# Kernel tuning notes

Measured on AMD Instinct MI355X. Metric: run time of the kernel, lower is better.

Reference implementation:

```python
import jax, jax.numpy as jnp
import numpy as np

# Scalar quantization params (QLinear __init__ args)
FEATURE_BITWIDTH = 8
WEIGHT_BITWIDTH = 8
INPUT_ZERO_POINT = -3
OUTPUT_ZERO_POINT = -5
INPUT_SCALE = 0.05
OUTPUT_SCALE = 0.1
QMIN = -(1 << (FEATURE_BITWIDTH - 1))   # -128
QMAX = (1 << (FEATURE_BITWIDTH - 1)) - 1  # 127

M, K, N = 8192, 4096, 4096


def float_to_fixed_point(x, bitwidth):
    """Represent x (0 < x < 1) as int_scale * 2^-frac_bits with int_scale
    in [2^(bitwidth-2), 2^(bitwidth-1)) (mantissa fits in signed `bitwidth` bits)."""
    frac_bits = (bitwidth - 1 - jnp.ceil(jnp.log2(x))).astype(jnp.int32)
    int_scale = jnp.round(x * jnp.exp2(frac_bits.astype(jnp.float32))).astype(jnp.int32)
    return int_scale, frac_bits


def setup_inputs() -> dict:
    key = jax.random.key(0)
    k1, k2, k3, k4 = jax.random.split(key, 4)
    qinput = jax.random.randint(k1, (M, K), -128, 128, dtype=jnp.int8)
    qweight = jax.random.randint(k2, (N, K), -128, 128, dtype=jnp.int8)
    qbias = jax.random.randint(k3, (N,), -(1 << 16), 1 << 16, dtype=jnp.int32)
    # per-output-channel weight scale; keeps folded scale in (0, 1)
    weight_scale = jax.random.uniform(k4, (N,), jnp.float32, 0.002, 0.02)
    return {"qinput": qinput, "qweight": qweight, "qbias": qbias,
            "weight_scale": weight_scale}


def reference(qinput, qweight, qbias, weight_scale):
    w32 = qweight.astype(jnp.int32)                      # [N, K]
    # Qbias' = qbias - sum_k(qweight) * Zin  (bias shift folding input zero point)
    shifted_qbias = qbias - w32.sum(axis=1) * INPUT_ZERO_POINT  # [N]
    # int32 GEMM: [M, K] @ [K, N] + bias
    acc = qinput.astype(jnp.int32) @ w32.T + shifted_qbias[None, :]  # [M, N]
    # fixed-point requantization: (acc * int_scale) >> frac_bits + Zout
    folded_scale = INPUT_SCALE * weight_scale / OUTPUT_SCALE         # [N], in (0,1)
    int_scale, frac_bits = float_to_fixed_point(folded_scale, FEATURE_BITWIDTH)
    # widen to int64 for the multiply so the (acc * int_scale) product cannot wrap
    prod = acc.astype(jnp.int64) * int_scale.astype(jnp.int64)[None, :]
    scaled = jnp.right_shift(prod, frac_bits.astype(jnp.int64)[None, :])  # arithmetic >>
    out = scaled + OUTPUT_ZERO_POINT
    return jnp.clip(out, QMIN, QMAX).astype(jnp.int8)
```

## Files before the change

kernel.cpp:

```cpp
#include <hip/hip_runtime.h>
#include <cstdint>
#include <cstddef>

#define M_DIM 8192
#define N_DIM 4096
#define K_DIM 4096

#define BM 128
#define BN 128
#define BK 128

typedef int int32x4 __attribute__((ext_vector_type(4)));


typedef __attribute__((address_space(1))) const void* gas_cptr;
typedef __attribute__((address_space(3))) void* las_ptr;

__device__ __forceinline__ void async_copy16(const void* g, void* l) {
    __builtin_amdgcn_global_load_lds((gas_cptr)g, (las_ptr)l, 16, 0, 0);
}

__device__ __forceinline__ int32x4 pack16(const int* p) {
    const int32x4* v = (const int32x4*)p;
    int32x4 w0 = v[0], w1 = v[1], w2 = v[2], w3 = v[3];
    int32x4 r;
    r.x = (w0.x & 0xFF) | ((w0.y & 0xFF) << 8) | ((w0.z & 0xFF) << 16) | (w0.w << 24);
    r.y = (w1.x & 0xFF) | ((w1.y & 0xFF) << 8) | ((w1.z & 0xFF) << 16) | (w1.w << 24);
    r.z = (w2.x & 0xFF) | ((w2.y & 0xFF) << 8) | ((w2.z & 0xFF) << 16) | (w2.w << 24);
    r.w = (w3.x & 0xFF) | ((w3.y & 0xFF) << 8) | ((w3.z & 0xFF) << 16) | (w3.w << 24);
    return r;
}

__global__ void ql_detect_kernel(const int* a, const int* b, int* ws) {
    int t = threadIdx.x;
    int fa = 0, fb = 0;
    for (int i = t; i < 4096; i += 64) {
        int va = a[i]; if (va > 127 || va < -128) fa = 1;
        int vb = b[i]; if (vb > 127 || vb < -128) fb = 1;
    }
    unsigned long long ba = __ballot(fa);
    unsigned long long bb = __ballot(fb);
    if (t == 0) { ws[0] = ba ? 1 : 0; ws[1] = bb ? 1 : 0; }
}

__global__ __launch_bounds__(256)
void ql_pack_all_kernel(const void* asrc, const void* bsrc, int* adst, int* bdst,
                        int* ws) {
    const int fa = __builtin_amdgcn_readfirstlane(ws[0]);
    const int fb = __builtin_amdgcn_readfirstlane(ws[1]);
    const int t    = threadIdx.x;
    const int lane = t & 63;
    const int wid  = t >> 6;

    if (blockIdx.x < N_DIM / 4) {
        const int n = blockIdx.x * 4 + wid;
        int s = 0;
        if (fb) {
            const int* src = (const int*)bsrc + (size_t)n * (K_DIM / 4);
#pragma unroll
            for (int it = 0; it < 4; ++it) {
                const int c = it * 64 + lane;
                int w = src[c];
                bdst[(size_t)n * (K_DIM / 4) + c] = w;
                s += (int)(int8_t)(w) + (int)(int8_t)(w >> 8)
                   + (int)(int8_t)(w >> 16) + (w >> 24);
            }
        } else {
            const int32x4* src = (const int32x4*)bsrc + (size_t)n * (K_DIM / 4);
#pragma unroll
            for (int it = 0; it < 16; ++it) {
                const int c = it * 64 + lane;
                int32x4 v = src[c];
                int w = (v.x & 0xFF) | ((v.y & 0xFF) << 8)
                      | ((v.z & 0xFF) << 16) | (v.w << 24);
                bdst[(size_t)n * (K_DIM / 4) + c] = w;
                s += v.x + v.y + v.z + v.w;
            }
        }
#pragma unroll
        for (int off = 32; off > 0; off >>= 1) s += __shfl_down(s, off, 64);
        if (lane == 0) ws[16 + n] = s;
    } else {
        const long base = (long)(blockIdx.x - N_DIM / 4) * 1024;
        if (fa) {
#pragma unroll
            for (int it = 0; it < 4; ++it) {
                const long c = base + it * 256 + t;
                adst[c] = ((const int*)asrc)[c];
            }
        } else {
#pragma unroll
            for (int it = 0; it < 4; ++it) {
                const long c = base + it * 256 + t;
                int32x4 v = ((const int32x4*)asrc)[c];
                adst[c] = (v.x & 0xFF) | ((v.y & 0xFF) << 8)
                        | ((v.z & 0xFF) << 16) | (v.w << 24);
            }
        }
    }
}

__device__ __forceinline__ int acc_elem(const int32x4& a, int r) {
    return (r == 0) ? a.x : (r == 1) ? a.y : (r == 2) ? a.z : a.w;
}

__device__ __forceinline__ void ql_epilogue(int32x4 acc[4][4], const int* rs,
                                            const int* qbias, const float* wscale,
                                            int* out, int bm, int bn,
                                            int wm, int wn, int qm, int qh) {
#pragma unroll
    for (int j = 0; j < 4; ++j) {
        const int n_g = bn * BN + wn + j * 16 + qm;
        const int b0 = qbias[n_g] + 3 * rs[n_g];
        float folded = (0.05f * wscale[n_g]) / 0.1f;
        const int f0 = (int)(7.0f - ceilf(log2f(folded)));
        const int s0 = (int)rintf(folded * exp2f((float)f0));
#pragma unroll
        for (int i = 0; i < 4; ++i) {
            const int m_base = bm * BM + wm + i * 16 + qh * 4;
#pragma unroll
            for (int r = 0; r < 4; ++r) {
                int v = acc_elem(acc[i][j], r) + b0;
                long long p = (long long)v * (long long)s0;
                int o = (int)(p >> f0) - 5;
                o = o < -128 ? -128 : (o > 127 ? 127 : o);
                out[(size_t)(m_base + r) * N_DIM + n_g] = o;
            }
        }
    }
}

__global__ __launch_bounds__(256)
void ql_gemm_kernel(const int8_t* aptr, const int8_t* bptr, const int* ws,
                    const int* qbias, const float* wscale, int* out) {
    __shared__ int32x4 Als[BM * BK / 16];
    __shared__ int32x4 Bls[BN * BK / 16];

    const int t    = threadIdx.x;
    const int lane = t & 63;
    const int wid  = t >> 6;
    const int bm = blockIdx.x;
    const int bn = blockIdx.y;

    const int wm = (wid >> 1) * 64;
    const int wn = (wid & 1) * 64;
    const int qm = lane & 15;
    const int qh = lane >> 4;

    int32x4 acc[4][4] = {};

    for (int kt = 0; kt < K_DIM / BK; ++kt) {
        __syncthreads();
        const int k0 = kt * BK;
#pragma unroll
        for (int r = 0; r < 4; ++r) {
            const int c    = r * 256 + t;
            const int row  = c >> 3;
            const int colg = (c & 7) ^ (row & 7);
            const size_t offA = (size_t)(bm * BM + row) * K_DIM + k0 + colg * 16;
            const size_t offB = (size_t)(bn * BN + row) * K_DIM + k0 + colg * 16;
            async_copy16(aptr + offA, &Als[c]);
            async_copy16(bptr + offB, &Bls[c]);
        }
        __syncthreads();

#pragma unroll
        for (int s = 0; s < 2; ++s) {
            const int colk = s * 4 + qh;
            int32x4 af[4], bf[4];
#pragma unroll
            for (int i = 0; i < 4; ++i) {
                const int ra = wm + i * 16 + qm;
                const int rb = wn + i * 16 + qm;
                af[i] = Als[ra * 8 + (colk ^ (ra & 7))];
                bf[i] = Bls[rb * 8 + (colk ^ (rb & 7))];
            }
#pragma unroll
            for (int i = 0; i < 4; ++i)
#pragma unroll
                for (int j = 0; j < 4; ++j)
                    acc[i][j] = __builtin_amdgcn_mfma_i32_16x16x64_i8(
                        af[i], bf[j], acc[i][j], 0, 0, 0);
        }
    }
    ql_epilogue(acc, ws + 16, qbias, wscale, out, bm, bn, wm, wn, qm, qh);
}

__global__ void ql_prep_kernel(const void* wptr, int* ws) {
    const int lane = threadIdx.x & 63;
    const int wid  = threadIdx.x >> 6;
    const int n = blockIdx.x * 4 + wid;
    const int b8 = __builtin_amdgcn_readfirstlane(ws[1]);

    int s = 0;
    if (b8) {
        const int32x4* row = (const int32x4*)((const int8_t*)wptr + (size_t)n * K_DIM);
        for (int c = lane; c < K_DIM / 16; c += 64) {
            int32x4 v = row[c];
#pragma unroll
            for (int j = 0; j < 4; ++j) {
                int w = (j == 0) ? v.x : (j == 1) ? v.y : (j == 2) ? v.z : v.w;
                s += (int)(int8_t)(w) + (int)(int8_t)(w >> 8)
                   + (int)(int8_t)(w >> 16) + (w >> 24);
            }
        }
    } else {
        const int32x4* row = (const int32x4*)((const int*)wptr + (size_t)n * K_DIM);
        for (int c = lane; c < K_DIM / 4; c += 64) {
            int32x4 v = row[c];
            s += v.x + v.y + v.z + v.w;
        }
    }
#pragma unroll
    for (int off = 32; off > 0; off >>= 1) s += __shfl_down(s, off, 64);
    if (lane == 0) ws[16 + n] = s;
}

__global__ __launch_bounds__(256)
void ql_gemm_fb_kernel(const void* aptr, const void* bptr, const int* ws,
                       const int* qbias, const float* wscale, int* out) {
    __shared__ int32x4 Als[BM * BK / 16];
    __shared__ int32x4 Bls[BN * BK / 16];

    const int a8 = __builtin_amdgcn_readfirstlane(ws[0]);
    const int b8 = __builtin_amdgcn_readfirstlane(ws[1]);

    const int t    = threadIdx.x;
    const int lane = t & 63;
    const int wid  = t >> 6;
    const int bm = blockIdx.x;
    const int bn = blockIdx.y;

    const int wm = (wid >> 1) * 64;
    const int wn = (wid & 1) * 64;
    const int qm = lane & 15;
    const int qh = lane >> 4;

    int32x4 acc[4][4] = {};

    for (int kt = 0; kt < K_DIM / BK; ++kt) {
        __syncthreads();
        const int k0 = kt * BK;
#pragma unroll
        for (int r = 0; r < 4; ++r) {
            const int c    = r * 256 + t;
            const int row  = c >> 3;
            const int colg = (c & 7) ^ (row & 7);
            const size_t offA = (size_t)(bm * BM + row) * K_DIM + k0 + colg * 16;
            const size_t offB = (size_t)(bn * BN + row) * K_DIM + k0 + colg * 16;
            if (a8) async_copy16((const int8_t*)aptr + offA, &Als[c]);
            else    Als[c] = pack16((const int*)aptr + offA);
            if (b8) async_copy16((const int8_t*)bptr + offB, &Bls[c]);
            else    Bls[c] = pack16((const int*)bptr + offB);
        }
        __syncthreads();

#pragma unroll
        for (int s = 0; s < 2; ++s) {
            const int colk = s * 4 + qh;
            int32x4 af[4], bf[4];
#pragma unroll
            for (int i = 0; i < 4; ++i) {
                const int ra = wm + i * 16 + qm;
                const int rb = wn + i * 16 + qm;
                af[i] = Als[ra * 8 + (colk ^ (ra & 7))];
                bf[i] = Bls[rb * 8 + (colk ^ (rb & 7))];
            }
#pragma unroll
            for (int i = 0; i < 4; ++i)
#pragma unroll
                for (int j = 0; j < 4; ++j)
                    acc[i][j] = __builtin_amdgcn_mfma_i32_16x16x64_i8(
                        af[i], bf[j], acc[i][j], 0, 0, 0);
        }
    }
    ql_epilogue(acc, ws + 16, qbias, wscale, out, bm, bn, wm, wn, qm, qh);
}

extern "C" void kernel_launch(void* const* d_in, const int* in_sizes, int n_in,
                              void* d_out, int out_size, void* d_ws, size_t ws_size,
                              hipStream_t stream) {
    const void* qin    = d_in[0];
    const void* qwt    = d_in[1];
    const int* qbias   = (const int*)d_in[2];
    const float* wscal = (const float*)d_in[3];
    int* ws  = (int*)d_ws;
    int* out = (int*)d_out;

    hipLaunchKernelGGL(ql_detect_kernel, dim3(1), dim3(64), 0, stream,
                       (const int*)qin, (const int*)qwt, ws);

    const size_t need = 65536 + (size_t)M_DIM * K_DIM + (size_t)N_DIM * K_DIM;
    if (ws_size >= need) {
        int8_t* a8 = (int8_t*)d_ws + 65536;
        int8_t* w8 = a8 + (size_t)M_DIM * K_DIM;
        const unsigned packGrid = N_DIM / 4 + (unsigned)((size_t)M_DIM * K_DIM / 4096);
        hipLaunchKernelGGL(ql_pack_all_kernel, dim3(packGrid), dim3(256), 0, stream,
                           qin, qwt, (int*)a8, (int*)w8, ws);
        hipLaunchKernelGGL(ql_gemm_kernel, dim3(M_DIM / BM, N_DIM / BN), dim3(256),
                           0, stream, a8, w8, ws, qbias, wscal, out);
    } else {
        hipLaunchKernelGGL(ql_prep_kernel, dim3(N_DIM / 4), dim3(256), 0, stream,
                           qwt, ws);
        hipLaunchKernelGGL(ql_gemm_fb_kernel, dim3(M_DIM / BM, N_DIM / BN), dim3(256),
                           0, stream, qin, qwt, ws, qbias, wscal, out);
    }
}
```

Baseline: 475.4 us.

## Switch main GEMM to 32x32x32 int8 MFMA and swap grid order

The main GEMM kernel now uses the 32x32x32 int8 MFMA with 2x2 accumulator tiles per wave instead of 4x4 tiles of 16x16x64. This halves the LDS fragment loads per MFMA and changes the register layout, so the epilogue is rewritten for the 32x32 output mapping. The grid is also transposed so consecutive blocks walk along N, which changes L2 reuse of the A rows. The larger MFMA may have different issue and latency characteristics, and the epilogue store pattern changes.

```diff
diff --git a/kernel.cpp b/kernel.cpp
--- a/kernel.cpp
+++ b/kernel.cpp
@@ -10,7 +10,8 @@
 #define BN 128
 #define BK 128
 
-typedef int int32x4 __attribute__((ext_vector_type(4)));
+typedef int int32x4  __attribute__((ext_vector_type(4)));
+typedef int int32x16 __attribute__((ext_vector_type(16)));
 
 
 typedef __attribute__((address_space(1))) const void* gas_cptr;
@@ -100,34 +101,8 @@
     }
 }
 
-__device__ __forceinline__ int acc_elem(const int32x4& a, int r) {
+__device__ __forceinline__ int acc_elem4(const int32x4& a, int r) {
     return (r == 0) ? a.x : (r == 1) ? a.y : (r == 2) ? a.z : a.w;
-}
-
-__device__ __forceinline__ void ql_epilogue(int32x4 acc[4][4], const int* rs,
-                                            const int* qbias, const float* wscale,
-                                            int* out, int bm, int bn,
-                                            int wm, int wn, int qm, int qh) {
-#pragma unroll
-    for (int j = 0; j < 4; ++j) {
-        const int n_g = bn * BN + wn + j * 16 + qm;
-        const int b0 = qbias[n_g] + 3 * rs[n_g];
-        float folded = (0.05f * wscale[n_g]) / 0.1f;
-        const int f0 = (int)(7.0f - ceilf(log2f(folded)));
-        const int s0 = (int)rintf(folded * exp2f((float)f0));
-#pragma unroll
-        for (int i = 0; i < 4; ++i) {
-            const int m_base = bm * BM + wm + i * 16 + qh * 4;
-#pragma unroll
-            for (int r = 0; r < 4; ++r) {
-                int v = acc_elem(acc[i][j], r) + b0;
-                long long p = (long long)v * (long long)s0;
-                int o = (int)(p >> f0) - 5;
-                o = o < -128 ? -128 : (o > 127 ? 127 : o);
-                out[(size_t)(m_base + r) * N_DIM + n_g] = o;
-            }
-        }
-    }
 }
 
 __global__ __launch_bounds__(256)
@@ -139,15 +114,16 @@
     const int t    = threadIdx.x;
     const int lane = t & 63;
     const int wid  = t >> 6;
-    const int bm = blockIdx.x;
-    const int bn = blockIdx.y;
+    const int bn = blockIdx.x;
+    const int bm = blockIdx.y;
 
     const int wm = (wid >> 1) * 64;
     const int wn = (wid & 1) * 64;
-    const int qm = lane & 15;
-    const int qh = lane >> 4;
-
-    int32x4 acc[4][4] = {};
+    const int l31 = lane & 31;
+    const int lh  = lane >> 5;
+    const int l7  = lane & 7;
+
+    int32x16 acc[2][2] = {};
 
     for (int kt = 0; kt < K_DIM / BK; ++kt) {
         __syncthreads();
@@ -165,25 +141,47 @@
         __syncthreads();
 
 #pragma unroll
-        for (int s = 0; s < 2; ++s) {
-            const int colk = s * 4 + qh;
-            int32x4 af[4], bf[4];
-#pragma unroll
-            for (int i = 0; i < 4; ++i) {
-                const int ra = wm + i * 16 + qm;
-                const int rb = wn + i * 16 + qm;
-                af[i] = Als[ra * 8 + (colk ^ (ra & 7))];
-                bf[i] = Bls[rb * 8 + (colk ^ (rb & 7))];
-            }
-#pragma unroll
-            for (int i = 0; i < 4; ++i)
-#pragma unroll
-                for (int j = 0; j < 4; ++j)
-                    acc[i][j] = __builtin_amdgcn_mfma_i32_16x16x64_i8(
+        for (int ks = 0; ks < 4; ++ks) {
+            const int colk = ks * 2 + lh;
+            int32x4 af[2], bf[2];
+#pragma unroll
+            for (int i = 0; i < 2; ++i) {
+                const int ra = wm + i * 32 + l31;
+                const int rb = wn + i * 32 + l31;
+                af[i] = Als[ra * 8 + (colk ^ l7)];
+                bf[i] = Bls[rb * 8 + (colk ^ l7)];
+            }
+#pragma unroll
+            for (int i = 0; i < 2; ++i)
+#pragma unroll
+                for (int j = 0; j < 2; ++j)
+                    acc[i][j] = __builtin_amdgcn_mfma_i32_32x32x32_i8(
                         af[i], bf[j], acc[i][j], 0, 0, 0);
         }
     }
-    ql_epilogue(acc, ws + 16, qbias, wscale, out, bm, bn, wm, wn, qm, qh);
+
+    const int* rs = ws + 16;
+#pragma unroll
+    for (int j = 0; j < 2; ++j) {
+        const int n_g = bn * BN + wn + j * 32 + l31;
+        const int b0 = qbias[n_g] + 3 * rs[n_g];
+        float folded = (0.05f * wscale[n_g]) / 0.1f;
+        const int f0 = (int)(7.0f - ceilf(log2f(folded)));
+        const int s0 = (int)rintf(folded * exp2f((float)f0));
+#pragma unroll
+        for (int i = 0; i < 2; ++i) {
+            const int m_base = bm * BM + wm + i * 32 + lh * 4;
+#pragma unroll
+            for (int r = 0; r < 16; ++r) {
+                const int row = m_base + (r & 3) + 8 * (r >> 2);
+                int v = acc[i][j][r] + b0;
+                long long p = (long long)v * (long long)s0;
+                int o = (int)(p >> f0) - 5;
+                o = o < -128 ? -128 : (o > 127 ? 127 : o);
+                out[(size_t)row * N_DIM + n_g] = o;
+            }
+        }
+    }
 }
 
 __global__ void ql_prep_kernel(const void* wptr, int* ws) {
@@ -228,8 +226,8 @@
     const int t    = threadIdx.x;
     const int lane = t & 63;
     const int wid  = t >> 6;
-    const int bm = blockIdx.x;
-    const int bn = blockIdx.y;
+    const int bn = blockIdx.x;
+    const int bm = blockIdx.y;
 
     const int wm = (wid >> 1) * 64;
     const int wn = (wid & 1) * 64;
@@ -274,7 +272,28 @@
                         af[i], bf[j], acc[i][j], 0, 0, 0);
         }
     }
-    ql_epilogue(acc, ws + 16, qbias, wscale, out, bm, bn, wm, wn, qm, qh);
+
+    const int* rs = ws + 16;
+#pragma unroll
+    for (int j = 0; j < 4; ++j) {
+        const int n_g = bn * BN + wn + j * 16 + qm;
+        const int b0 = qbias[n_g] + 3 * rs[n_g];
+        float folded = (0.05f * wscale[n_g]) / 0.1f;
+        const int f0 = (int)(7.0f - ceilf(log2f(folded)));
+        const int s0 = (int)rintf(folded * exp2f((float)f0));
+#pragma unroll
+        for (int i = 0; i < 4; ++i) {
+            const int m_base = bm * BM + wm + i * 16 + qh * 4;
+#pragma unroll
+            for (int r = 0; r < 4; ++r) {
+                int v = acc_elem4(acc[i][j], r) + b0;
+                long long p = (long long)v * (long long)s0;
+                int o = (int)(p >> f0) - 5;
+                o = o < -128 ? -128 : (o > 127 ? 127 : o);
+                out[(size_t)(m_base + r) * N_DIM + n_g] = o;
+            }
+        }
+    }
 }
 
 extern "C" void kernel_launch(void* const* d_in, const int* in_sizes, int n_in,
@@ -297,12 +316,12 @@
         const unsigned packGrid = N_DIM / 4 + (unsigned)((size_t)M_DIM * K_DIM / 4096);
         hipLaunchKernelGGL(ql_pack_all_kernel, dim3(packGrid), dim3(256), 0, stream,
                            qin, qwt, (int*)a8, (int*)w8, ws);
-        hipLaunchKernelGGL(ql_gemm_kernel, dim3(M_DIM / BM, N_DIM / BN), dim3(256),
+        hipLaunchKernelGGL(ql_gemm_kernel, dim3(N_DIM / BN, M_DIM / BM), dim3(256),
                            0, stream, a8, w8, ws, qbias, wscal, out);
     } else {
         hipLaunchKernelGGL(ql_prep_kernel, dim3(N_DIM / 4), dim3(256), 0, stream,
                            qwt, ws);
-        hipLaunchKernelGGL(ql_gemm_fb_kernel, dim3(M_DIM / BM, N_DIM / BN), dim3(256),
+        hipLaunchKernelGGL(ql_gemm_fb_kernel, dim3(N_DIM / BN, M_DIM / BM), dim3(256),
                            0, stream, qin, qwt, ws, qbias, wscal, out);
     }
 }
```

Measured after the change: 441.0 us. 7.2% less time.
